# Performance work log

Measured on AMD Instinct MI355X. Metric: run time of the kernel, lower is better.

Reference implementation:

```python
import jax, jax.numpy as jnp
import numpy as np
import math

D_MODEL = 768
N_HEADS = 6
HD = D_MODEL // N_HEADS  # 128
RANK = D_MODEL // 4      # 192
B, T = 128, 256


def _rope_tables(T, dim):
    # matches torch: inv = 1/10000**(arange(0,dim,2)/dim); emb = cat([outer(t,inv)]*2, -1)
    inv = 1.0 / (10000.0 ** (jnp.arange(0, dim, 2, dtype=jnp.float32) / dim))
    t = jnp.arange(T, dtype=jnp.float32)
    freqs = jnp.outer(t, inv)                       # [T, dim/2]
    emb = jnp.concatenate([freqs, freqs], axis=-1)  # [T, dim]
    return jnp.cos(emb), jnp.sin(emb)               # each [T, dim]


def _rot(x):
    h = x.shape[-1] // 2
    return jnp.concatenate([-x[..., h:], x[..., :h]], axis=-1)


def setup_inputs() -> dict:
    key = jax.random.key(0)
    ks = jax.random.split(key, 8)
    s_in = 1.0 / math.sqrt(D_MODEL)
    s_r = 1.0 / math.sqrt(RANK)
    inp = {
        'x': jax.random.normal(ks[0], (B, T, D_MODEL), dtype=jnp.float32),
        'qA': jax.random.normal(ks[1], (D_MODEL, RANK), dtype=jnp.float32) * s_in,
        'qB': jax.random.normal(ks[2], (RANK, D_MODEL), dtype=jnp.float32) * s_r,
        'kA': jax.random.normal(ks[3], (D_MODEL, RANK), dtype=jnp.float32) * s_in,
        'kB': jax.random.normal(ks[4], (RANK, D_MODEL), dtype=jnp.float32) * s_r,
        'vA': jax.random.normal(ks[5], (D_MODEL, RANK), dtype=jnp.float32) * s_in,
        'vB': jax.random.normal(ks[6], (RANK, D_MODEL), dtype=jnp.float32) * s_r,
        'o_w': jax.random.normal(ks[7], (D_MODEL, D_MODEL), dtype=jnp.float32) * s_in,
    }
    return inp


def reference(x, qA, qB, kA, kB, vA, vB, o_w):
    Bb, Tt, _ = x.shape
    # low-rank projections: in -> rank -> out, then split heads [B, H, T, hd]
    def proj(A, W):
        h = (x @ A) @ W
        return h.reshape(Bb, Tt, N_HEADS, HD).transpose(0, 2, 1, 3)
    q = proj(qA, qB)
    k = proj(kA, kB)
    v = proj(vA, vB)
    cos, sin = _rope_tables(Tt, HD)  # [T, hd], broadcast over B, H
    q = q * cos + _rot(q) * sin
    k = k * cos + _rot(k) * sin
    att = jnp.einsum('bhqd,bhkd->bhqk', q, k) / math.sqrt(HD)
    causal = jnp.tril(jnp.ones((Tt, Tt), dtype=bool))
    att = jnp.where(causal, att, -jnp.inf)
    att = jax.nn.softmax(att, axis=-1)
    out = jnp.einsum('bhqk,bhkd->bhqd', att, v)          # [B, H, T, hd]
    out = out.transpose(0, 2, 1, 3).reshape(Bb, Tt, D_MODEL)
    return out @ o_w
```

## Files before the change

kernel.cpp:

```cpp
#include <hip/hip_runtime.h>
#include <hip/hip_bf16.h>
#include <stdint.h>

typedef __attribute__((ext_vector_type(8))) short s16x8;
typedef __attribute__((ext_vector_type(4))) float f32x4;

#define D_MODEL 768
#define N_HEADS 6
#define HD 128
#define RANK 192
#define TT 256
#define NROW 32768
#define QKV_LD 2304
#define NK 12
#define QSCL 0.08838834764831845f

__device__ inline short f2bf(float f) {
  union { float f; unsigned u; } x; x.f = f;
  unsigned r = x.u + 0x7fffu + ((x.u >> 16) & 1u);
  return (short)(r >> 16);
}
__device__ inline float bf2f(short v) {
  union { unsigned u; float f; } x; x.u = ((unsigned)(unsigned short)v) << 16;
  return x.f;
}
__device__ inline void gload_lds16(const void* g, void* lds) {
  __builtin_amdgcn_global_load_lds(
      (const __attribute__((address_space(1))) unsigned int*)g,
      (__attribute__((address_space(3))) unsigned int*)lds, 16, 0, 0);
}

#define BAR()    asm volatile("s_barrier" ::: "memory")
#define LGKM0()  asm volatile("s_waitcnt lgkmcnt(0)" ::: "memory")
#define WAITVM4() asm volatile("s_waitcnt vmcnt(4)" ::: "memory")
#define WAITVM0() asm volatile("s_waitcnt vmcnt(0)" ::: "memory")

#define NB_CAST 12288
#define NB_WOT  2304
#define NB_MAKEW 432
#define NB_TAB  64

__global__ void k_setup(const float* __restrict__ x, short* __restrict__ xb,
                        const float* __restrict__ ow,
                        const float* __restrict__ qA, const float* __restrict__ qB,
                        const float* __restrict__ kA, const float* __restrict__ kB,
                        const float* __restrict__ vA, const float* __restrict__ vB,
                        short* __restrict__ WT,
                        float* __restrict__ cosT, float* __restrict__ sinT) {
  const int bid = blockIdx.x, tid = threadIdx.x;
  if (bid < NB_CAST) {
    int t = bid * 256 + tid;
    const float4* xp = (const float4*)x;
    float4 a = xp[t * 2], b = xp[t * 2 + 1];
    s16x8 o;
    o[0] = f2bf(a.x); o[1] = f2bf(a.y); o[2] = f2bf(a.z); o[3] = f2bf(a.w);
    o[4] = f2bf(b.x); o[5] = f2bf(b.y); o[6] = f2bf(b.z); o[7] = f2bf(b.w);
    *(s16x8*)(xb + (size_t)t * 8) = o;
  } else if (bid < NB_CAST + NB_WOT) {
    int g = (bid - NB_CAST) * 256 + tid;
    int n = g % 768, kk = g / 768;
    WT[(size_t)(2304 + n) * 768 + kk] = f2bf(ow[(size_t)kk * 768 + n]);
  } else if (bid < NB_CAST + NB_WOT + NB_MAKEW) {
    int g = (bid - NB_CAST - NB_WOT) * 256 + tid;
    int n4 = g % 576, kkb = g / 576;
    int part = n4 / 192, nnb = (n4 % 192) * 4;
    const float* A = (part == 0) ? qA : (part == 1) ? kA : vA;
    const float* Bm = (part == 0) ? qB : (part == 1) ? kB : vB;
    float acc[4][4] = {};
    for (int r0 = 0; r0 < RANK; r0 += 4) {
      float4 a4[4], b4[4];
#pragma unroll
      for (int q = 0; q < 4; ++q)
        a4[q] = *(const float4*)&A[(kkb + q * 192) * RANK + r0];
#pragma unroll
      for (int i = 0; i < 4; ++i)
        b4[i] = *(const float4*)&Bm[(r0 + i) * 768 + nnb];
#pragma unroll
      for (int q = 0; q < 4; ++q) {
        const float* aq = (const float*)&a4[q];
#pragma unroll
        for (int i = 0; i < 4; ++i) {
          const float* bi = (const float*)&b4[i];
#pragma unroll
          for (int jn = 0; jn < 4; ++jn)
            acc[q][jn] += aq[i] * bi[jn];
        }
      }
    }
#pragma unroll
    for (int q = 0; q < 4; ++q)
#pragma unroll
      for (int jn = 0; jn < 4; ++jn)
        WT[(size_t)(part * 768 + nnb + jn) * 768 + kkb + q * 192] = f2bf(acc[q][jn]);
  } else {
    int t2 = (bid - NB_CAST - NB_WOT - NB_MAKEW) * 256 + tid;
    int t = t2 >> 6, i = t2 & 63;
    float inv = powf(10000.0f, -(float)i / 64.0f);
    float ang = (float)t * inv;
    cosT[t2] = cosf(ang);
    sinT[t2] = sinf(ang);
  }
}

__device__ inline s16x8 rdfrag(const short* hbase, int rowbyte, int ksl4x, int swz) {
  return *(const s16x8*)((const char*)hbase + rowbyte + (((ksl4x) ^ (swz)) << 4));
}

template <bool OUTBF>
__global__ __launch_bounds__(512, 2) void k_gemm8(const short* __restrict__ A,
                                                  const short* __restrict__ Bt,
                                                  void* __restrict__ Cv, int ldc) {
  extern __shared__ short lds[];
  const int tid = threadIdx.x;
  const int wid = tid >> 6, lane = tid & 63;
  const int l15 = lane & 15, l4 = lane >> 4;
  const int wr = wid >> 2, wc = wid & 3;
  const int swz = l15 & 7;
  const int bid = blockIdx.y * 128 + blockIdx.x;
  const int nper = gridDim.y;
  const int xcd = bid & 7, loc = bid >> 3;
  const int mq = loc / nper;
  const int mt = xcd * 16 + mq;
  const int nt = loc - mq * nper;
  const long mbase = (long)mt * 256;
  const long nbase = (long)nt * 256;

  const int hb0 = wid * 2048 + lane * 16;
  const int hb1 = hb0 + 1024;
  const int r0 = hb0 >> 7, c0 = ((hb0 >> 4) & 7) ^ (r0 & 7);
  const int r1 = hb1 >> 7, c1 = ((hb1 >> 4) & 7) ^ (r1 & 7);
  const int off0 = r0 * 768 + c0 * 8;
  const int off1 = r1 * 768 + c1 * 8;

#define STAGE(G, rowoff, kt, ldsS) do {                                        \
    gload_lds16((G) + (size_t)(rowoff) * 768 + (kt) * 64 + off0,               \
                (char*)(ldsS) + wid * 2048);                                   \
    gload_lds16((G) + (size_t)(rowoff) * 768 + (kt) * 64 + off1,               \
                (char*)(ldsS) + wid * 2048 + 1024);                            \
  } while (0)

#define LDSA(buf, half) (lds + ((buf) * 2 + (half)) * 8192)
#define LDSB(buf, half) (lds + 32768 + ((buf) * 2 + (half)) * 8192)

  f32x4 acc[8][4] = {};

  STAGE(A,  mbase,       0, LDSA(0, 0));
  STAGE(Bt, nbase,       0, LDSB(0, 0));
  STAGE(A,  mbase + 128, 0, LDSA(0, 1));
  STAGE(Bt, nbase + 128, 0, LDSB(0, 1));
  STAGE(A,  mbase,       1, LDSA(1, 0));
  STAGE(Bt, nbase,       1, LDSB(1, 0));
  WAITVM4();
  BAR();

  s16x8 a03[4][2], a47[4][2], b01[2][2], b23[2][2];

#pragma unroll
  for (int kt = 0; kt < NK; ++kt) {
    const int buf = kt & 1, nbuf = buf ^ 1;
    const short* Ab = LDSA(buf, wr);
    const short* Bb = LDSB(buf, (wc >> 1));
    const int browbase = (wc & 1) * 64 * 128;

#pragma unroll
    for (int mf = 0; mf < 4; ++mf)
#pragma unroll
      for (int ks = 0; ks < 2; ++ks)
        a03[mf][ks] = rdfrag(Ab, (mf * 16 + l15) * 128, ks * 4 + l4, swz);
#pragma unroll
    for (int nf = 0; nf < 2; ++nf)
#pragma unroll
      for (int ks = 0; ks < 2; ++ks)
        b01[nf][ks] = rdfrag(Bb, browbase + (nf * 16 + l15) * 128, ks * 4 + l4, swz);
    if (kt + 1 < NK) STAGE(A, mbase + 128, kt + 1, LDSA(nbuf, 1));
    BAR();
    LGKM0();
    __builtin_amdgcn_s_setprio(1);
#pragma unroll
    for (int mf = 0; mf < 4; ++mf)
#pragma unroll
      for (int nf = 0; nf < 2; ++nf)
#pragma unroll
        for (int ks = 0; ks < 2; ++ks)
          acc[mf][nf] = __builtin_amdgcn_mfma_f32_16x16x32_bf16(a03[mf][ks], b01[nf][ks], acc[mf][nf], 0, 0, 0);
    __builtin_amdgcn_s_setprio(0);
    BAR();

#pragma unroll
    for (int mf = 0; mf < 4; ++mf)
#pragma unroll
      for (int ks = 0; ks < 2; ++ks)
        a47[mf][ks] = rdfrag(Ab, ((mf + 4) * 16 + l15) * 128, ks * 4 + l4, swz);
    if (kt + 1 < NK) STAGE(Bt, nbase + 128, kt + 1, LDSB(nbuf, 1));
    BAR();
    LGKM0();
    __builtin_amdgcn_s_setprio(1);
#pragma unroll
    for (int mf = 0; mf < 4; ++mf)
#pragma unroll
      for (int nf = 0; nf < 2; ++nf)
#pragma unroll
        for (int ks = 0; ks < 2; ++ks)
          acc[mf + 4][nf] = __builtin_amdgcn_mfma_f32_16x16x32_bf16(a47[mf][ks], b01[nf][ks], acc[mf + 4][nf], 0, 0, 0);
    __builtin_amdgcn_s_setprio(0);
    BAR();

#pragma unroll
    for (int nf = 0; nf < 2; ++nf)
#pragma unroll
      for (int ks = 0; ks < 2; ++ks)
        b23[nf][ks] = rdfrag(Bb, browbase + ((nf + 2) * 16 + l15) * 128, ks * 4 + l4, swz);
    if (kt + 2 < NK) STAGE(A, mbase, kt + 2, LDSA(buf, 0));
    BAR();
    LGKM0();
    __builtin_amdgcn_s_setprio(1);
#pragma unroll
    for (int mf = 0; mf < 4; ++mf)
#pragma unroll
      for (int nf = 0; nf < 2; ++nf)
#pragma unroll
        for (int ks = 0; ks < 2; ++ks)
          acc[mf][nf + 2] = __builtin_amdgcn_mfma_f32_16x16x32_bf16(a03[mf][ks], b23[nf][ks], acc[mf][nf + 2], 0, 0, 0);
    __builtin_amdgcn_s_setprio(0);
    BAR();

    if (kt + 2 < NK) STAGE(Bt, nbase, kt + 2, LDSB(buf, 0));
    BAR();
    __builtin_amdgcn_s_setprio(1);
#pragma unroll
    for (int mf = 0; mf < 4; ++mf)
#pragma unroll
      for (int nf = 0; nf < 2; ++nf)
#pragma unroll
        for (int ks = 0; ks < 2; ++ks)
          acc[mf + 4][nf + 2] = __builtin_amdgcn_mfma_f32_16x16x32_bf16(a47[mf][ks], b23[nf][ks], acc[mf + 4][nf + 2], 0, 0, 0);
    __builtin_amdgcn_s_setprio(0);
    if (kt < NK - 1) {
      if (kt + 2 < NK) WAITVM4(); else WAITVM0();
      BAR();
    }
  }
#undef STAGE

#pragma unroll
  for (int mf = 0; mf < 8; ++mf)
#pragma unroll
    for (int nf = 0; nf < 4; ++nf)
#pragma unroll
      for (int r = 0; r < 4; ++r) {
        long row = mbase + wr * 128 + mf * 16 + l4 * 4 + r;
        long col = nbase + wc * 64 + nf * 16 + l15;
        if (OUTBF) ((short*)Cv)[row * ldc + col] = f2bf(acc[mf][nf][r]);
        else       ((float*)Cv)[row * ldc + col] = acc[mf][nf][r];
      }
}

__global__ void k_ropek(short* __restrict__ qkv, const float* __restrict__ cosT,
                        const float* __restrict__ sinT) {
  int tid = blockIdx.x * 256 + threadIdx.x;
  int row = tid / 48, rem = tid % 48;
  int head = rem >> 3, i8 = (rem & 7) * 8;
  int t = row & (TT - 1);
  size_t base = (size_t)row * QKV_LD + D_MODEL + head * 128 + i8;
  s16x8 a = *(const s16x8*)(qkv + base);
  s16x8 b = *(const s16x8*)(qkv + base + 64);
  const float4* cp = (const float4*)(cosT + t * 64 + i8);
  const float4* sp = (const float4*)(sinT + t * 64 + i8);
  float4 c04 = cp[0], c14 = cp[1], s04 = sp[0], s14 = sp[1];
  float cs[8] = {c04.x, c04.y, c04.z, c04.w, c14.x, c14.y, c14.z, c14.w};
  float sn[8] = {s04.x, s04.y, s04.z, s04.w, s14.x, s14.y, s14.z, s14.w};
  s16x8 na, nb;
#pragma unroll
  for (int j = 0; j < 8; ++j) {
    float av = bf2f(a[j]), bv = bf2f(b[j]);
    na[j] = f2bf(av * cs[j] - bv * sn[j]);
    nb[j] = f2bf(bv * cs[j] + av * sn[j]);
  }
  *(s16x8*)(qkv + base) = na;
  *(s16x8*)(qkv + base + 64) = nb;
}

__global__ __launch_bounds__(512) void k_attn(const short* __restrict__ qkv,
                                              short* __restrict__ attout,
                                              const float* __restrict__ cosT,
                                              const float* __restrict__ sinT) {
  extern __shared__ short smem[];
  short* Kls0 = smem;
  short* Kls1 = smem + 8192;
  short* Vt   = smem + 16384;
  const int tid = threadIdx.x;
  const int wid = tid >> 6, lane = tid & 63;
  const int l15 = lane & 15, l4 = lane >> 4;
  short* PlsW = smem + 24576 + wid * 2048;
  const int b = blockIdx.x / N_HEADS, h = blockIdx.x % N_HEADS;
  const long row0 = (long)b * TT;
  const int d0 = wid * 16;
  const int rb[2] = {wid, 15 - wid};

  s16x8 qf[2][4];
#pragma unroll
  for (int mi = 0; mi < 2; ++mi)
#pragma unroll
    for (int kc = 0; kc < 4; ++kc) {
      long row = row0 + rb[mi] * 16 + l15;
      qf[mi][kc] = *(const s16x8*)(qkv + row * QKV_LD + h * HD + kc * 32 + l4 * 8);
    }
#pragma unroll
  for (int mi = 0; mi < 2; ++mi) {
    int t = rb[mi] * 16 + l15;
#pragma unroll
    for (int kc = 0; kc < 2; ++kc) {
      const float4* cp = (const float4*)(cosT + t * 64 + kc * 32 + l4 * 8);
      const float4* sp = (const float4*)(sinT + t * 64 + kc * 32 + l4 * 8);
      float4 c04 = cp[0], c14 = cp[1], s04 = sp[0], s14 = sp[1];
      float cs[8] = {c04.x, c04.y, c04.z, c04.w, c14.x, c14.y, c14.z, c14.w};
      float sn[8] = {s04.x, s04.y, s04.z, s04.w, s14.x, s14.y, s14.z, s14.w};
#pragma unroll
      for (int jj = 0; jj < 8; ++jj) {
        float av = bf2f(qf[mi][kc][jj]);
        float bv = bf2f(qf[mi][kc + 2][jj]);
        qf[mi][kc][jj]     = f2bf((av * cs[jj] - bv * sn[jj]) * QSCL);
        qf[mi][kc + 2][jj] = f2bf((bv * cs[jj] + av * sn[jj]) * QSCL);
      }
    }
  }

#define STAGEK(j_, Kd) do {                                                     \
    int bb0_ = wid * 2048 + lane * 16;                                          \
    int r0_ = bb0_ >> 8; int sc0_ = ((bb0_ >> 4) & 15) ^ (r0_ & 7);             \
    gload_lds16(qkv + (row0 + (j_) * 64 + r0_) * QKV_LD + D_MODEL + h * HD + sc0_ * 8, \
                (char*)(Kd) + wid * 2048);                                      \
    int bb1_ = bb0_ + 1024;                                                     \
    int r1_ = bb1_ >> 8; int sc1_ = ((bb1_ >> 4) & 15) ^ (r1_ & 7);             \
    gload_lds16(qkv + (row0 + (j_) * 64 + r1_) * QKV_LD + D_MODEL + h * HD + sc1_ * 8, \
                (char*)(Kd) + wid * 2048 + 1024);                               \
  } while (0)

#define LOADV(j_, va, vb) do {                                                  \
    const short* vsrc_ = qkv + (row0 + (j_) * 64 + lane) * QKV_LD + 2 * D_MODEL + h * HD + d0; \
    va = *(const s16x8*)vsrc_;                                                  \
    vb = *(const s16x8*)(vsrc_ + 8);                                            \
  } while (0)

  float mst[2][4], lst[2][4];
  f32x4 oacc[2][8];
#pragma unroll
  for (int mi = 0; mi < 2; ++mi)
#pragma unroll
    for (int r = 0; r < 4; ++r) { mst[mi][r] = -1e30f; lst[mi][r] = 0.f; }
#pragma unroll
  for (int mi = 0; mi < 2; ++mi)
#pragma unroll
    for (int nd = 0; nd < 8; ++nd) oacc[mi][nd] = {0.f, 0.f, 0.f, 0.f};

  const int jmax = (15 - wid) >> 2;

  STAGEK(0, Kls0);
  s16x8 vr[2][2];
  LOADV(0, vr[0][0], vr[0][1]);

#pragma unroll
  for (int j = 0; j < 4; ++j) {
    const int buf = j & 1;
    const short* Kb = buf ? Kls1 : Kls0;
    short* Kn = buf ? Kls0 : Kls1;
    if (j < 3) {
      STAGEK(j + 1, Kn);
      LOADV(j + 1, vr[buf ^ 1][0], vr[buf ^ 1][1]);
    }
    if (j < 3) WAITVM4(); else WAITVM0();
    __builtin_amdgcn_sched_barrier(0);
    BAR();
#pragma unroll
    for (int e = 0; e < 8; ++e)
      *(short*)((char*)Vt + (d0 + e) * 128 + (((lane >> 3) ^ e) << 4) + (lane & 7) * 2) = vr[buf][0][e];
#pragma unroll
    for (int e = 0; e < 8; ++e)
      *(short*)((char*)Vt + (d0 + 8 + e) * 128 + (((lane >> 3) ^ e) << 4) + (lane & 7) * 2) = vr[buf][1][e];

    if (j <= jmax) {
      f32x4 sacc[2][4] = {};
#pragma unroll
      for (int kc = 0; kc < 4; ++kc) {
        s16x8 kf[4];
#pragma unroll
        for (int ni = 0; ni < 4; ++ni)
          kf[ni] = *(const s16x8*)((const char*)Kb + (ni * 16 + l15) * 256 +
                                   (((kc * 4 + l4) ^ (l15 & 7)) << 4));
#pragma unroll
        for (int mi = 0; mi < 2; ++mi)
#pragma unroll
          for (int ni = 0; ni < 4; ++ni)
            sacc[mi][ni] = __builtin_amdgcn_mfma_f32_16x16x32_bf16(qf[mi][kc], kf[ni], sacc[mi][ni], 0, 0, 0);
      }
#pragma unroll
      for (int mi = 0; mi < 2; ++mi) {
#pragma unroll
        for (int r = 0; r < 4; ++r) {
          int qr = rb[mi] * 16 + l4 * 4 + r;
          float rm = -1e30f;
#pragma unroll
          for (int ni = 0; ni < 4; ++ni) {
            int kvc = j * 64 + ni * 16 + l15;
            if (kvc > qr) sacc[mi][ni][r] = -1e30f;
            rm = fmaxf(rm, sacc[mi][ni][r]);
          }
#pragma unroll
          for (int d2 = 1; d2 < 16; d2 <<= 1)
            rm = fmaxf(rm, __shfl_xor(rm, d2, 64));
          float mold = mst[mi][r];
          float mnew = fmaxf(mold, rm);
          float alpha = __expf(mold - mnew);
          mst[mi][r] = mnew;
          float rs = 0.f;
#pragma unroll
          for (int ni = 0; ni < 4; ++ni) {
            float p = __expf(sacc[mi][ni][r] - mnew);
            sacc[mi][ni][r] = p;
            rs += p;
          }
#pragma unroll
          for (int d2 = 1; d2 < 16; d2 <<= 1)
            rs += __shfl_xor(rs, d2, 64);
          lst[mi][r] = lst[mi][r] * alpha + rs;
#pragma unroll
          for (int nd = 0; nd < 8; ++nd)
            oacc[mi][nd][r] *= alpha;
        }
      }
#pragma unroll
      for (int mi = 0; mi < 2; ++mi)
#pragma unroll
        for (int ni = 0; ni < 4; ++ni)
#pragma unroll
          for (int r = 0; r < 4; ++r) {
            int prow = mi * 16 + l4 * 4 + r;
            int pcp = (ni * 2 + (l15 >> 3)) ^ (prow & 7);
            *(short*)((char*)PlsW + prow * 128 + (pcp << 4) + (l15 & 7) * 2) =
                f2bf(sacc[mi][ni][r]);
          }
    }
    LGKM0();
    BAR();
    __builtin_amdgcn_sched_barrier(0);
    if (j <= jmax) {
#pragma unroll
      for (int kc2 = 0; kc2 < 2; ++kc2) {
        s16x8 pa[2];
#pragma unroll
        for (int mi = 0; mi < 2; ++mi)
          pa[mi] = *(const s16x8*)((const char*)PlsW + (mi * 16 + l15) * 128 +
                                   (((kc2 * 4 + l4) ^ (l15 & 7)) << 4));
#pragma unroll
        for (int nd = 0; nd < 8; ++nd) {
          s16x8 vf = *(const s16x8*)((const char*)Vt + (nd * 16 + l15) * 128 +
                                     (((kc2 * 4 + l4) ^ (l15 & 7)) << 4));
#pragma unroll
          for (int mi = 0; mi < 2; ++mi)
            oacc[mi][nd] = __builtin_amdgcn_mfma_f32_16x16x32_bf16(pa[mi], vf, oacc[mi][nd], 0, 0, 0);
        }
      }
    }
  }
#undef STAGEK
#undef LOADV
#pragma unroll
  for (int mi = 0; mi < 2; ++mi)
#pragma unroll
    for (int nd = 0; nd < 8; ++nd)
#pragma unroll
      for (int r = 0; r < 4; ++r) {
        long row = row0 + rb[mi] * 16 + l4 * 4 + r;
        int col = h * HD + nd * 16 + l15;
        attout[row * D_MODEL + col] = f2bf(oacc[mi][nd][r] / lst[mi][r]);
      }
}

extern "C" void kernel_launch(void* const* d_in, const int* in_sizes, int n_in,
                              void* d_out, int out_size, void* d_ws, size_t ws_size,
                              hipStream_t stream) {
  const float* x  = (const float*)d_in[0];
  const float* qA = (const float*)d_in[1];
  const float* qB = (const float*)d_in[2];
  const float* kA = (const float*)d_in[3];
  const float* kB = (const float*)d_in[4];
  const float* vA = (const float*)d_in[5];
  const float* vB = (const float*)d_in[6];
  const float* ow = (const float*)d_in[7];

  char* ws = (char*)d_ws;
  short* qkv   = (short*)ws;
  short* xb    = (short*)(ws + 150994944);
  short* WT    = (short*)(ws + 201326592);
  float* cosT  = (float*)(ws + 206045184);
  float* sinT  = (float*)(ws + 206110720);
  short* attout = xb;

  hipFuncSetAttribute((const void*)k_gemm8<true>,
                      hipFuncAttributeMaxDynamicSharedMemorySize, 131072);
  hipFuncSetAttribute((const void*)k_gemm8<false>,
                      hipFuncAttributeMaxDynamicSharedMemorySize, 131072);
  hipFuncSetAttribute((const void*)k_attn,
                      hipFuncAttributeMaxDynamicSharedMemorySize, 81920);

  k_setup<<<NB_CAST + NB_WOT + NB_MAKEW + NB_TAB, 256, 0, stream>>>(
      x, xb, ow, qA, qB, kA, kB, vA, vB, WT, cosT, sinT);
  k_gemm8<true><<<dim3(128, 9), 512, 131072, stream>>>(xb, WT, (void*)qkv, QKV_LD);
  k_ropek<<<6144, 256, 0, stream>>>(qkv, cosT, sinT);
  k_attn<<<768, 512, 81920, stream>>>(qkv, attout, cosT, sinT);
  k_gemm8<false><<<dim3(128, 3), 512, 131072, stream>>>(attout, WT + (size_t)2304 * 768, d_out, 768);
}
```

Baseline: 384.1 us.

## Fuse RoPE and Q scaling into the QKV GEMM epilogue via interleaved weight columns

Within each head, the Q and K weight columns are permuted so every rotary pair sits in adjacent columns. The QKV GEMM epilogue then applies RoPE with a lane shuffle and folds the softmax scale into Q. This removes the separate k_ropek pass over K and the in-attention Q rotation. The same permutation applied to Q and K leaves their dot products unchanged. The attention kernel also remaps each wave's query row blocks from a balanced (w, 15-w) pairing to contiguous (2w, 2w+1), which may unbalance causal work across waves.

```diff
diff --git a/kernel.cpp b/kernel.cpp
--- a/kernel.cpp
+++ b/kernel.cpp
@@ -90,8 +90,16 @@
 #pragma unroll
     for (int q = 0; q < 4; ++q)
 #pragma unroll
-      for (int jn = 0; jn < 4; ++jn)
-        WT[(size_t)(part * 768 + nnb + jn) * 768 + kkb + q * 192] = f2bf(acc[q][jn]);
+      for (int jn = 0; jn < 4; ++jn) {
+        int nl = nnb + jn;
+        int np = nl;
+        if (part < 2) {
+          int hh = nl >> 7, ii = nl & 127;
+          int pi = (ii < 64) ? (2 * ii) : (2 * (ii - 64) + 1);
+          np = hh * 128 + pi;
+        }
+        WT[(size_t)(part * 768 + np) * 768 + kkb + q * 192] = f2bf(acc[q][jn]);
+      }
   } else {
     int t2 = (bid - NB_CAST - NB_WOT - NB_MAKEW) * 256 + tid;
     int t = t2 >> 6, i = t2 & 63;
@@ -106,10 +114,12 @@
   return *(const s16x8*)((const char*)hbase + rowbyte + (((ksl4x) ^ (swz)) << 4));
 }
 
-template <bool OUTBF>
+template <bool OUTBF, bool ROPE>
 __global__ __launch_bounds__(512, 2) void k_gemm8(const short* __restrict__ A,
                                                   const short* __restrict__ Bt,
-                                                  void* __restrict__ Cv, int ldc) {
+                                                  void* __restrict__ Cv, int ldc,
+                                                  const float* __restrict__ cosT,
+                                                  const float* __restrict__ sinT) {
   extern __shared__ short lds[];
   const int tid = threadIdx.x;
   const int wid = tid >> 6, lane = tid & 63;
@@ -245,45 +255,34 @@
 #pragma unroll
   for (int mf = 0; mf < 8; ++mf)
 #pragma unroll
-    for (int nf = 0; nf < 4; ++nf)
+    for (int nf = 0; nf < 4; ++nf) {
+      const long col = nbase + wc * 64 + nf * 16 + l15;
+      const int ci = (int)col;
+      const bool dorope = ROPE && (ci < 1536);
+      const float scl = (ci < 768) ? QSCL : 1.0f;
+      const int freq = (ci & 127) >> 1;
+      const bool odd = (ci & 1);
 #pragma unroll
       for (int r = 0; r < 4; ++r) {
         long row = mbase + wr * 128 + mf * 16 + l4 * 4 + r;
-        long col = nbase + wc * 64 + nf * 16 + l15;
-        if (OUTBF) ((short*)Cv)[row * ldc + col] = f2bf(acc[mf][nf][r]);
-        else       ((float*)Cv)[row * ldc + col] = acc[mf][nf][r];
-      }
-}
-
-__global__ void k_ropek(short* __restrict__ qkv, const float* __restrict__ cosT,
-                        const float* __restrict__ sinT) {
-  int tid = blockIdx.x * 256 + threadIdx.x;
-  int row = tid / 48, rem = tid % 48;
-  int head = rem >> 3, i8 = (rem & 7) * 8;
-  int t = row & (TT - 1);
-  size_t base = (size_t)row * QKV_LD + D_MODEL + head * 128 + i8;
-  s16x8 a = *(const s16x8*)(qkv + base);
-  s16x8 b = *(const s16x8*)(qkv + base + 64);
-  const float4* cp = (const float4*)(cosT + t * 64 + i8);
-  const float4* sp = (const float4*)(sinT + t * 64 + i8);
-  float4 c04 = cp[0], c14 = cp[1], s04 = sp[0], s14 = sp[1];
-  float cs[8] = {c04.x, c04.y, c04.z, c04.w, c14.x, c14.y, c14.z, c14.w};
-  float sn[8] = {s04.x, s04.y, s04.z, s04.w, s14.x, s14.y, s14.z, s14.w};
-  s16x8 na, nb;
-#pragma unroll
-  for (int j = 0; j < 8; ++j) {
-    float av = bf2f(a[j]), bv = bf2f(b[j]);
-    na[j] = f2bf(av * cs[j] - bv * sn[j]);
-    nb[j] = f2bf(bv * cs[j] + av * sn[j]);
-  }
-  *(s16x8*)(qkv + base) = na;
-  *(s16x8*)(qkv + base + 64) = nb;
+        float v = acc[mf][nf][r];
+        if (ROPE) {
+          float p = __shfl_xor(v, 1, 64);
+          if (dorope) {
+            int t = (int)(row & (TT - 1));
+            float c = cosT[t * 64 + freq], s = sinT[t * 64 + freq];
+            v = odd ? (v * c + p * s) : (v * c - p * s);
+            v *= scl;
+          }
+        }
+        if (OUTBF) ((short*)Cv)[row * ldc + col] = f2bf(v);
+        else       ((float*)Cv)[row * ldc + col] = v;
+      }
+    }
 }
 
 __global__ __launch_bounds__(512) void k_attn(const short* __restrict__ qkv,
-                                              short* __restrict__ attout,
-                                              const float* __restrict__ cosT,
-                                              const float* __restrict__ sinT) {
+                                              short* __restrict__ attout) {
   extern __shared__ short smem[];
   short* Kls0 = smem;
   short* Kls1 = smem + 8192;
@@ -295,7 +294,7 @@
   const int b = blockIdx.x / N_HEADS, h = blockIdx.x % N_HEADS;
   const long row0 = (long)b * TT;
   const int d0 = wid * 16;
-  const int rb[2] = {wid, 15 - wid};
+  const int rb[2] = {2 * wid, 2 * wid + 1};
 
   s16x8 qf[2][4];
 #pragma unroll
@@ -305,25 +304,6 @@
       long row = row0 + rb[mi] * 16 + l15;
       qf[mi][kc] = *(const s16x8*)(qkv + row * QKV_LD + h * HD + kc * 32 + l4 * 8);
     }
-#pragma unroll
-  for (int mi = 0; mi < 2; ++mi) {
-    int t = rb[mi] * 16 + l15;
-#pragma unroll
-    for (int kc = 0; kc < 2; ++kc) {
-      const float4* cp = (const float4*)(cosT + t * 64 + kc * 32 + l4 * 8);
-      const float4* sp = (const float4*)(sinT + t * 64 + kc * 32 + l4 * 8);
-      float4 c04 = cp[0], c14 = cp[1], s04 = sp[0], s14 = sp[1];
-      float cs[8] = {c04.x, c04.y, c04.z, c04.w, c14.x, c14.y, c14.z, c14.w};
-      float sn[8] = {s04.x, s04.y, s04.z, s04.w, s14.x, s14.y, s14.z, s14.w};
-#pragma unroll
-      for (int jj = 0; jj < 8; ++jj) {
-        float av = bf2f(qf[mi][kc][jj]);
-        float bv = bf2f(qf[mi][kc + 2][jj]);
-        qf[mi][kc][jj]     = f2bf((av * cs[jj] - bv * sn[jj]) * QSCL);
-        qf[mi][kc + 2][jj] = f2bf((bv * cs[jj] + av * sn[jj]) * QSCL);
-      }
-    }
-  }
 
 #define STAGEK(j_, Kd) do {                                                     \
     int bb0_ = wid * 2048 + lane * 16;                                          \
@@ -353,7 +333,7 @@
 #pragma unroll
     for (int nd = 0; nd < 8; ++nd) oacc[mi][nd] = {0.f, 0.f, 0.f, 0.f};
 
-  const int jmax = (15 - wid) >> 2;
+  const int jmax = (2 * wid + 1) >> 2;
 
   STAGEK(0, Kls0);
   s16x8 vr[2][2];
@@ -496,17 +476,18 @@
   float* sinT  = (float*)(ws + 206110720);
   short* attout = xb;
 
-  hipFuncSetAttribute((const void*)k_gemm8<true>,
+  hipFuncSetAttribute((const void*)k_gemm8<true, true>,
                       hipFuncAttributeMaxDynamicSharedMemorySize, 131072);
-  hipFuncSetAttribute((const void*)k_gemm8<false>,
+  hipFuncSetAttribute((const void*)k_gemm8<false, false>,
                       hipFuncAttributeMaxDynamicSharedMemorySize, 131072);
   hipFuncSetAttribute((const void*)k_attn,
                       hipFuncAttributeMaxDynamicSharedMemorySize, 81920);
 
   k_setup<<<NB_CAST + NB_WOT + NB_MAKEW + NB_TAB, 256, 0, stream>>>(
       x, xb, ow, qA, qB, kA, kB, vA, vB, WT, cosT, sinT);
-  k_gemm8<true><<<dim3(128, 9), 512, 131072, stream>>>(xb, WT, (void*)qkv, QKV_LD);
-  k_ropek<<<6144, 256, 0, stream>>>(qkv, cosT, sinT);
-  k_attn<<<768, 512, 81920, stream>>>(qkv, attout, cosT, sinT);
-  k_gemm8<false><<<dim3(128, 3), 512, 131072, stream>>>(attout, WT + (size_t)2304 * 768, d_out, 768);
-}
+  k_gemm8<true, true><<<dim3(128, 9), 512, 131072, stream>>>(
+      xb, WT, (void*)qkv, QKV_LD, cosT, sinT);
+  k_attn<<<768, 512, 81920, stream>>>(qkv, attout);
+  k_gemm8<false, false><<<dim3(128, 3), 512, 131072, stream>>>(
+      attout, WT + (size_t)2304 * 768, d_out, 768, cosT, sinT);
+}
```

Result: slower. 445.3 us (+15.9%).

## Halve GEMM K-tile to 32 and use contiguous query-row blocks per attention wave

Applied to the files above, without the earlier changes.

The GEMM kernel now stages 32-wide K slices instead of 64, doubling the number of K iterations. This halves LDS use per block (64KB instead of 128KB) and changes the swizzle to suit 64-byte rows, aiming for higher occupancy or less LDS pressure. The attention kernel now gives each wave a contiguous 32-row query block rather than the paired balanced blocks (wid, 15-wid). Under the causal mask this unbalances work across waves, with late waves doing more KV tiles, which may lengthen block runtime.

```diff
diff --git a/kernel.cpp b/kernel.cpp
--- a/kernel.cpp
+++ b/kernel.cpp
@@ -12,7 +12,7 @@
 #define TT 256
 #define NROW 32768
 #define QKV_LD 2304
-#define NK 12
+#define NK 24
 #define QSCL 0.08838834764831845f
 
 __device__ inline short f2bf(float f) {
@@ -32,6 +32,7 @@
 
 #define BAR()    asm volatile("s_barrier" ::: "memory")
 #define LGKM0()  asm volatile("s_waitcnt lgkmcnt(0)" ::: "memory")
+#define WAITVM2() asm volatile("s_waitcnt vmcnt(2)" ::: "memory")
 #define WAITVM4() asm volatile("s_waitcnt vmcnt(4)" ::: "memory")
 #define WAITVM0() asm volatile("s_waitcnt vmcnt(0)" ::: "memory")
 
@@ -102,10 +103,6 @@
   }
 }
 
-__device__ inline s16x8 rdfrag(const short* hbase, int rowbyte, int ksl4x, int swz) {
-  return *(const s16x8*)((const char*)hbase + rowbyte + (((ksl4x) ^ (swz)) << 4));
-}
-
 template <bool OUTBF>
 __global__ __launch_bounds__(512, 2) void k_gemm8(const short* __restrict__ A,
                                                   const short* __restrict__ Bt,
@@ -115,7 +112,7 @@
   const int wid = tid >> 6, lane = tid & 63;
   const int l15 = lane & 15, l4 = lane >> 4;
   const int wr = wid >> 2, wc = wid & 3;
-  const int swz = l15 & 7;
+  const int swz = (l15 >> 1) & 3;
   const int bid = blockIdx.y * 128 + blockIdx.x;
   const int nper = gridDim.y;
   const int xcd = bid & 7, loc = bid >> 3;
@@ -125,22 +122,16 @@
   const long mbase = (long)mt * 256;
   const long nbase = (long)nt * 256;
 
-  const int hb0 = wid * 2048 + lane * 16;
-  const int hb1 = hb0 + 1024;
-  const int r0 = hb0 >> 7, c0 = ((hb0 >> 4) & 7) ^ (r0 & 7);
-  const int r1 = hb1 >> 7, c1 = ((hb1 >> 4) & 7) ^ (r1 & 7);
-  const int off0 = r0 * 768 + c0 * 8;
-  const int off1 = r1 * 768 + c1 * 8;
-
-#define STAGE(G, rowoff, kt, ldsS) do {                                        \
-    gload_lds16((G) + (size_t)(rowoff) * 768 + (kt) * 64 + off0,               \
-                (char*)(ldsS) + wid * 2048);                                   \
-    gload_lds16((G) + (size_t)(rowoff) * 768 + (kt) * 64 + off1,               \
-                (char*)(ldsS) + wid * 2048 + 1024);                            \
-  } while (0)
-
-#define LDSA(buf, half) (lds + ((buf) * 2 + (half)) * 8192)
-#define LDSB(buf, half) (lds + 32768 + ((buf) * 2 + (half)) * 8192)
+  const int sr = tid >> 2;
+  const int sc = (tid & 3) ^ ((sr >> 1) & 3);
+  const int soff = sr * 768 + sc * 8;
+
+#define STAGE(G, rowoff, kt, ldsS) \
+    gload_lds16((G) + (size_t)(rowoff) * 768 + (kt) * 32 + soff, \
+                (char*)(ldsS) + wid * 1024)
+
+#define LDSA(buf, half) (lds + ((buf) * 2 + (half)) * 4096)
+#define LDSB(buf, half) (lds + 16384 + ((buf) * 2 + (half)) * 4096)
 
   f32x4 acc[8][4] = {};
 
@@ -150,28 +141,24 @@
   STAGE(Bt, nbase + 128, 0, LDSB(0, 1));
   STAGE(A,  mbase,       1, LDSA(1, 0));
   STAGE(Bt, nbase,       1, LDSB(1, 0));
-  WAITVM4();
+  WAITVM2();
   BAR();
 
-  s16x8 a03[4][2], a47[4][2], b01[2][2], b23[2][2];
+  s16x8 a03[4], a47[4], b01[2], b23[2];
 
 #pragma unroll
   for (int kt = 0; kt < NK; ++kt) {
     const int buf = kt & 1, nbuf = buf ^ 1;
     const short* Ab = LDSA(buf, wr);
     const short* Bb = LDSB(buf, (wc >> 1));
-    const int browbase = (wc & 1) * 64 * 128;
-
-#pragma unroll
-    for (int mf = 0; mf < 4; ++mf)
-#pragma unroll
-      for (int ks = 0; ks < 2; ++ks)
-        a03[mf][ks] = rdfrag(Ab, (mf * 16 + l15) * 128, ks * 4 + l4, swz);
+    const int browbase = (wc & 1) * 64 * 64;
+
+#pragma unroll
+    for (int mf = 0; mf < 4; ++mf)
+      a03[mf] = *(const s16x8*)((const char*)Ab + (mf * 16 + l15) * 64 + ((l4 ^ swz) << 4));
 #pragma unroll
     for (int nf = 0; nf < 2; ++nf)
-#pragma unroll
-      for (int ks = 0; ks < 2; ++ks)
-        b01[nf][ks] = rdfrag(Bb, browbase + (nf * 16 + l15) * 128, ks * 4 + l4, swz);
+      b01[nf] = *(const s16x8*)((const char*)Bb + browbase + (nf * 16 + l15) * 64 + ((l4 ^ swz) << 4));
     if (kt + 1 < NK) STAGE(A, mbase + 128, kt + 1, LDSA(nbuf, 1));
     BAR();
     LGKM0();
@@ -180,17 +167,13 @@
     for (int mf = 0; mf < 4; ++mf)
 #pragma unroll
       for (int nf = 0; nf < 2; ++nf)
-#pragma unroll
-        for (int ks = 0; ks < 2; ++ks)
-          acc[mf][nf] = __builtin_amdgcn_mfma_f32_16x16x32_bf16(a03[mf][ks], b01[nf][ks], acc[mf][nf], 0, 0, 0);
+        acc[mf][nf] = __builtin_amdgcn_mfma_f32_16x16x32_bf16(a03[mf], b01[nf], acc[mf][nf], 0, 0, 0);
     __builtin_amdgcn_s_setprio(0);
     BAR();
 
 #pragma unroll
     for (int mf = 0; mf < 4; ++mf)
-#pragma unroll
-      for (int ks = 0; ks < 2; ++ks)
-        a47[mf][ks] = rdfrag(Ab, ((mf + 4) * 16 + l15) * 128, ks * 4 + l4, swz);
+      a47[mf] = *(const s16x8*)((const char*)Ab + ((mf + 4) * 16 + l15) * 64 + ((l4 ^ swz) << 4));
     if (kt + 1 < NK) STAGE(Bt, nbase + 128, kt + 1, LDSB(nbuf, 1));
     BAR();
     LGKM0();
@@ -199,17 +182,13 @@
     for (int mf = 0; mf < 4; ++mf)
 #pragma unroll
       for (int nf = 0; nf < 2; ++nf)
-#pragma unroll
-        for (int ks = 0; ks < 2; ++ks)
-          acc[mf + 4][nf] = __builtin_amdgcn_mfma_f32_16x16x32_bf16(a47[mf][ks], b01[nf][ks], acc[mf + 4][nf], 0, 0, 0);
+        acc[mf + 4][nf] = __builtin_amdgcn_mfma_f32_16x16x32_bf16(a47[mf], b01[nf], acc[mf + 4][nf], 0, 0, 0);
     __builtin_amdgcn_s_setprio(0);
     BAR();
 
 #pragma unroll
     for (int nf = 0; nf < 2; ++nf)
-#pragma unroll
-      for (int ks = 0; ks < 2; ++ks)
-        b23[nf][ks] = rdfrag(Bb, browbase + ((nf + 2) * 16 + l15) * 128, ks * 4 + l4, swz);
+      b23[nf] = *(const s16x8*)((const char*)Bb + browbase + ((nf + 2) * 16 + l15) * 64 + ((l4 ^ swz) << 4));
     if (kt + 2 < NK) STAGE(A, mbase, kt + 2, LDSA(buf, 0));
     BAR();
     LGKM0();
@@ -218,9 +197,7 @@
     for (int mf = 0; mf < 4; ++mf)
 #pragma unroll
       for (int nf = 0; nf < 2; ++nf)
-#pragma unroll
-        for (int ks = 0; ks < 2; ++ks)
-          acc[mf][nf + 2] = __builtin_amdgcn_mfma_f32_16x16x32_bf16(a03[mf][ks], b23[nf][ks], acc[mf][nf + 2], 0, 0, 0);
+        acc[mf][nf + 2] = __builtin_amdgcn_mfma_f32_16x16x32_bf16(a03[mf], b23[nf], acc[mf][nf + 2], 0, 0, 0);
     __builtin_amdgcn_s_setprio(0);
     BAR();
 
@@ -231,12 +208,10 @@
     for (int mf = 0; mf < 4; ++mf)
 #pragma unroll
       for (int nf = 0; nf < 2; ++nf)
-#pragma unroll
-        for (int ks = 0; ks < 2; ++ks)
-          acc[mf + 4][nf + 2] = __builtin_amdgcn_mfma_f32_16x16x32_bf16(a47[mf][ks], b23[nf][ks], acc[mf + 4][nf + 2], 0, 0, 0);
+        acc[mf + 4][nf + 2] = __builtin_amdgcn_mfma_f32_16x16x32_bf16(a47[mf], b23[nf], acc[mf + 4][nf + 2], 0, 0, 0);
     __builtin_amdgcn_s_setprio(0);
     if (kt < NK - 1) {
-      if (kt + 2 < NK) WAITVM4(); else WAITVM0();
+      if (kt + 2 < NK) WAITVM2(); else WAITVM0();
       BAR();
     }
   }
@@ -295,19 +270,18 @@
   const int b = blockIdx.x / N_HEADS, h = blockIdx.x % N_HEADS;
   const long row0 = (long)b * TT;
   const int d0 = wid * 16;
-  const int rb[2] = {wid, 15 - wid};
 
   s16x8 qf[2][4];
 #pragma unroll
   for (int mi = 0; mi < 2; ++mi)
 #pragma unroll
     for (int kc = 0; kc < 4; ++kc) {
-      long row = row0 + rb[mi] * 16 + l15;
+      long row = row0 + wid * 32 + mi * 16 + l15;
       qf[mi][kc] = *(const s16x8*)(qkv + row * QKV_LD + h * HD + kc * 32 + l4 * 8);
     }
 #pragma unroll
   for (int mi = 0; mi < 2; ++mi) {
-    int t = rb[mi] * 16 + l15;
+    int t = wid * 32 + mi * 16 + l15;
 #pragma unroll
     for (int kc = 0; kc < 2; ++kc) {
       const float4* cp = (const float4*)(cosT + t * 64 + kc * 32 + l4 * 8);
@@ -353,7 +327,7 @@
 #pragma unroll
     for (int nd = 0; nd < 8; ++nd) oacc[mi][nd] = {0.f, 0.f, 0.f, 0.f};
 
-  const int jmax = (15 - wid) >> 2;
+  const int jmax = (wid * 32 + 31) / 64;
 
   STAGEK(0, Kls0);
   s16x8 vr[2][2];
@@ -397,7 +371,7 @@
       for (int mi = 0; mi < 2; ++mi) {
 #pragma unroll
         for (int r = 0; r < 4; ++r) {
-          int qr = rb[mi] * 16 + l4 * 4 + r;
+          int qr = wid * 32 + mi * 16 + l4 * 4 + r;
           float rm = -1e30f;
 #pragma unroll
           for (int ni = 0; ni < 4; ++ni) {
@@ -470,7 +444,7 @@
     for (int nd = 0; nd < 8; ++nd)
 #pragma unroll
       for (int r = 0; r < 4; ++r) {
-        long row = row0 + rb[mi] * 16 + l4 * 4 + r;
+        long row = row0 + wid * 32 + mi * 16 + l4 * 4 + r;
         int col = h * HD + nd * 16 + l15;
         attout[row * D_MODEL + col] = f2bf(oacc[mi][nd][r] / lst[mi][r]);
       }
@@ -497,16 +471,16 @@
   short* attout = xb;
 
   hipFuncSetAttribute((const void*)k_gemm8<true>,
-                      hipFuncAttributeMaxDynamicSharedMemorySize, 131072);
+                      hipFuncAttributeMaxDynamicSharedMemorySize, 65536);
   hipFuncSetAttribute((const void*)k_gemm8<false>,
-                      hipFuncAttributeMaxDynamicSharedMemorySize, 131072);
+                      hipFuncAttributeMaxDynamicSharedMemorySize, 65536);
   hipFuncSetAttribute((const void*)k_attn,
                       hipFuncAttributeMaxDynamicSharedMemorySize, 81920);
 
   k_setup<<<NB_CAST + NB_WOT + NB_MAKEW + NB_TAB, 256, 0, stream>>>(
       x, xb, ow, qA, qB, kA, kB, vA, vB, WT, cosT, sinT);
-  k_gemm8<true><<<dim3(128, 9), 512, 131072, stream>>>(xb, WT, (void*)qkv, QKV_LD);
+  k_gemm8<true><<<dim3(128, 9), 512, 65536, stream>>>(xb, WT, (void*)qkv, QKV_LD);
   k_ropek<<<6144, 256, 0, stream>>>(qkv, cosT, sinT);
   k_attn<<<768, 512, 81920, stream>>>(qkv, attout, cosT, sinT);
-  k_gemm8<false><<<dim3(128, 3), 512, 131072, stream>>>(attout, WT + (size_t)2304 * 768, d_out, 768);
-}
+  k_gemm8<false><<<dim3(128, 3), 512, 65536, stream>>>(attout, WT + (size_t)2304 * 768, d_out, 768);
+}
```

Result: slower. 394.4 us (+2.7%).

## Split attention blocks into query halves with 4 waves each

Applied to the files above, without the earlier changes.

Each (batch, head) attention block is split into two blocks of 256 threads. Each block handles 128 query rows, 32 contiguous rows per wave, and the first half iterates over only 2 key tiles instead of 4. The change removes causal work from the early-query blocks and doubles the block count, which should improve load balance and occupancy with smaller LDS use. The cost is that K and V tiles are loaded twice for the shared prefix, and per-wave load imbalance rises because the mirrored row pairing is gone.

```diff
diff --git a/kernel.cpp b/kernel.cpp
--- a/kernel.cpp
+++ b/kernel.cpp
@@ -33,6 +33,7 @@
 #define BAR()    asm volatile("s_barrier" ::: "memory")
 #define LGKM0()  asm volatile("s_waitcnt lgkmcnt(0)" ::: "memory")
 #define WAITVM4() asm volatile("s_waitcnt vmcnt(4)" ::: "memory")
+#define WAITVM8() asm volatile("s_waitcnt vmcnt(8)" ::: "memory")
 #define WAITVM0() asm volatile("s_waitcnt vmcnt(0)" ::: "memory")
 
 #define NB_CAST 12288
@@ -280,7 +281,7 @@
   *(s16x8*)(qkv + base + 64) = nb;
 }
 
-__global__ __launch_bounds__(512) void k_attn(const short* __restrict__ qkv,
+__global__ __launch_bounds__(256) void k_attn(const short* __restrict__ qkv,
                                               short* __restrict__ attout,
                                               const float* __restrict__ cosT,
                                               const float* __restrict__ sinT) {
@@ -292,22 +293,25 @@
   const int wid = tid >> 6, lane = tid & 63;
   const int l15 = lane & 15, l4 = lane >> 4;
   short* PlsW = smem + 24576 + wid * 2048;
-  const int b = blockIdx.x / N_HEADS, h = blockIdx.x % N_HEADS;
+  const int bh = blockIdx.x >> 1, half = blockIdx.x & 1;
+  const int b = bh / N_HEADS, h = bh % N_HEADS;
   const long row0 = (long)b * TT;
-  const int d0 = wid * 16;
-  const int rb[2] = {wid, 15 - wid};
+  const int qbase = half * 128 + wid * 32;
+  const int d0 = wid * 32;
+  const int nt = half ? 4 : 2;
+  const int jmaxw = (qbase + 31) >> 6;
 
   s16x8 qf[2][4];
 #pragma unroll
   for (int mi = 0; mi < 2; ++mi)
 #pragma unroll
     for (int kc = 0; kc < 4; ++kc) {
-      long row = row0 + rb[mi] * 16 + l15;
+      long row = row0 + qbase + mi * 16 + l15;
       qf[mi][kc] = *(const s16x8*)(qkv + row * QKV_LD + h * HD + kc * 32 + l4 * 8);
     }
 #pragma unroll
   for (int mi = 0; mi < 2; ++mi) {
-    int t = rb[mi] * 16 + l15;
+    int t = qbase + mi * 16 + l15;
 #pragma unroll
     for (int kc = 0; kc < 2; ++kc) {
       const float4* cp = (const float4*)(cosT + t * 64 + kc * 32 + l4 * 8);
@@ -326,20 +330,19 @@
   }
 
 #define STAGEK(j_, Kd) do {                                                     \
-    int bb0_ = wid * 2048 + lane * 16;                                          \
-    int r0_ = bb0_ >> 8; int sc0_ = ((bb0_ >> 4) & 15) ^ (r0_ & 7);             \
-    gload_lds16(qkv + (row0 + (j_) * 64 + r0_) * QKV_LD + D_MODEL + h * HD + sc0_ * 8, \
-                (char*)(Kd) + wid * 2048);                                      \
-    int bb1_ = bb0_ + 1024;                                                     \
-    int r1_ = bb1_ >> 8; int sc1_ = ((bb1_ >> 4) & 15) ^ (r1_ & 7);             \
-    gload_lds16(qkv + (row0 + (j_) * 64 + r1_) * QKV_LD + D_MODEL + h * HD + sc1_ * 8, \
-                (char*)(Kd) + wid * 2048 + 1024);                               \
+    _Pragma("unroll")                                                           \
+    for (int q2 = 0; q2 < 4; ++q2) {                                            \
+      int bb_ = wid * 4096 + q2 * 1024 + lane * 16;                             \
+      int r_ = bb_ >> 8; int sc_ = ((bb_ >> 4) & 15) ^ (r_ & 7);                \
+      gload_lds16(qkv + (row0 + (j_) * 64 + r_) * QKV_LD + D_MODEL + h * HD + sc_ * 8, \
+                  (char*)(Kd) + wid * 4096 + q2 * 1024);                        \
+    }                                                                           \
   } while (0)
 
-#define LOADV(j_, va, vb) do {                                                  \
+#define LOADV(j_, vv) do {                                                      \
     const short* vsrc_ = qkv + (row0 + (j_) * 64 + lane) * QKV_LD + 2 * D_MODEL + h * HD + d0; \
-    va = *(const s16x8*)vsrc_;                                                  \
-    vb = *(const s16x8*)(vsrc_ + 8);                                            \
+    vv[0] = *(const s16x8*)vsrc_;       vv[1] = *(const s16x8*)(vsrc_ + 8);     \
+    vv[2] = *(const s16x8*)(vsrc_ + 16); vv[3] = *(const s16x8*)(vsrc_ + 24);   \
   } while (0)
 
   float mst[2][4], lst[2][4];
@@ -353,32 +356,30 @@
 #pragma unroll
     for (int nd = 0; nd < 8; ++nd) oacc[mi][nd] = {0.f, 0.f, 0.f, 0.f};
 
-  const int jmax = (15 - wid) >> 2;
-
   STAGEK(0, Kls0);
-  s16x8 vr[2][2];
-  LOADV(0, vr[0][0], vr[0][1]);
+  s16x8 vr[2][4];
+  LOADV(0, vr[0]);
 
 #pragma unroll
   for (int j = 0; j < 4; ++j) {
+    if (j >= nt) break;
     const int buf = j & 1;
     const short* Kb = buf ? Kls1 : Kls0;
     short* Kn = buf ? Kls0 : Kls1;
-    if (j < 3) {
+    if (j < nt - 1) {
       STAGEK(j + 1, Kn);
-      LOADV(j + 1, vr[buf ^ 1][0], vr[buf ^ 1][1]);
-    }
-    if (j < 3) WAITVM4(); else WAITVM0();
+      LOADV(j + 1, vr[buf ^ 1]);
+    }
+    if (j < nt - 1) WAITVM8(); else WAITVM0();
     __builtin_amdgcn_sched_barrier(0);
     BAR();
 #pragma unroll
-    for (int e = 0; e < 8; ++e)
-      *(short*)((char*)Vt + (d0 + e) * 128 + (((lane >> 3) ^ e) << 4) + (lane & 7) * 2) = vr[buf][0][e];
-#pragma unroll
-    for (int e = 0; e < 8; ++e)
-      *(short*)((char*)Vt + (d0 + 8 + e) * 128 + (((lane >> 3) ^ e) << 4) + (lane & 7) * 2) = vr[buf][1][e];
-
-    if (j <= jmax) {
+    for (int q = 0; q < 4; ++q)
+#pragma unroll
+      for (int e = 0; e < 8; ++e)
+        *(short*)((char*)Vt + (d0 + q * 8 + e) * 128 + (((lane >> 3) ^ e) << 4) + (lane & 7) * 2) = vr[buf][q][e];
+
+    if (j <= jmaxw) {
       f32x4 sacc[2][4] = {};
 #pragma unroll
       for (int kc = 0; kc < 4; ++kc) {
@@ -397,7 +398,7 @@
       for (int mi = 0; mi < 2; ++mi) {
 #pragma unroll
         for (int r = 0; r < 4; ++r) {
-          int qr = rb[mi] * 16 + l4 * 4 + r;
+          int qr = qbase + mi * 16 + l4 * 4 + r;
           float rm = -1e30f;
 #pragma unroll
           for (int ni = 0; ni < 4; ++ni) {
@@ -443,7 +444,7 @@
     LGKM0();
     BAR();
     __builtin_amdgcn_sched_barrier(0);
-    if (j <= jmax) {
+    if (j <= jmaxw) {
 #pragma unroll
       for (int kc2 = 0; kc2 < 2; ++kc2) {
         s16x8 pa[2];
@@ -470,7 +471,7 @@
     for (int nd = 0; nd < 8; ++nd)
 #pragma unroll
       for (int r = 0; r < 4; ++r) {
-        long row = row0 + rb[mi] * 16 + l4 * 4 + r;
+        long row = row0 + qbase + mi * 16 + l4 * 4 + r;
         int col = h * HD + nd * 16 + l15;
         attout[row * D_MODEL + col] = f2bf(oacc[mi][nd][r] / lst[mi][r]);
       }
@@ -501,12 +502,12 @@
   hipFuncSetAttribute((const void*)k_gemm8<false>,
                       hipFuncAttributeMaxDynamicSharedMemorySize, 131072);
   hipFuncSetAttribute((const void*)k_attn,
-                      hipFuncAttributeMaxDynamicSharedMemorySize, 81920);
+                      hipFuncAttributeMaxDynamicSharedMemorySize, 65536);
 
   k_setup<<<NB_CAST + NB_WOT + NB_MAKEW + NB_TAB, 256, 0, stream>>>(
       x, xb, ow, qA, qB, kA, kB, vA, vB, WT, cosT, sinT);
   k_gemm8<true><<<dim3(128, 9), 512, 131072, stream>>>(xb, WT, (void*)qkv, QKV_LD);
   k_ropek<<<6144, 256, 0, stream>>>(qkv, cosT, sinT);
-  k_attn<<<768, 512, 81920, stream>>>(qkv, attout, cosT, sinT);
+  k_attn<<<1536, 256, 65536, stream>>>(qkv, attout, cosT, sinT);
   k_gemm8<false><<<dim3(128, 3), 512, 131072, stream>>>(attout, WT + (size_t)2304 * 768, d_out, 768);
 }
```

Result: slower. 458.7 us (+19.4%).
